# Optimization experiments

Hardware: AMD Instinct MI355X
Metric: run time of the kernel (lower is better)

The kernel has to match this reference:

```python
import jax, jax.numpy as jnp
import numpy as np

D_MODEL = 1024
NUM_HEADS = 16
D_HEAD = D_MODEL // NUM_HEADS
THETA = 10000.0
NEG_INF = -1e9


def apply_rope(x, theta=THETA):
    # x: (..., S, Dh) with interleaved pairs (2i, 2i+1)
    S, Dh = x.shape[-2], x.shape[-1]
    inv_freq = 1.0 / (theta ** (jnp.arange(0, Dh, 2, dtype=jnp.float32) / Dh))  # (Dh/2,)
    ang = jnp.arange(S, dtype=jnp.float32)[:, None] * inv_freq[None, :]          # (S, Dh/2)
    cos, sin = jnp.cos(ang), jnp.sin(ang)
    x1 = x[..., 0::2]
    x2 = x[..., 1::2]
    r1 = x1 * cos - x2 * sin
    r2 = x1 * sin + x2 * cos
    # interleave back
    return jnp.stack([r1, r2], axis=-1).reshape(x.shape)


def setup_inputs() -> dict:
    key = jax.random.key(0)
    ks = jax.random.split(key, 5)
    B, S = 2, 2048
    scale = 1.0 / np.sqrt(D_MODEL)
    return {
        "x": jax.random.normal(ks[0], (B, S, D_MODEL), dtype=jnp.float32),
        "Wq": jax.random.normal(ks[1], (D_MODEL, D_MODEL), dtype=jnp.float32) * scale,
        "Wk": jax.random.normal(ks[2], (D_MODEL, D_MODEL), dtype=jnp.float32) * scale,
        "Wv": jax.random.normal(ks[3], (D_MODEL, D_MODEL), dtype=jnp.float32) * scale,
        "Wo": jax.random.normal(ks[4], (D_MODEL, D_MODEL), dtype=jnp.float32) * scale,
    }


def reference(x, Wq, Wk, Wv, Wo):
    B, S, _ = x.shape
    def split_heads(t):
        return t.reshape(B, S, NUM_HEADS, D_HEAD).transpose(0, 2, 1, 3)  # (B,H,S,Dh)
    # nn.Linear(bias=False): y = x @ W.T
    Q = split_heads(x @ Wq.T)
    K = split_heads(x @ Wk.T)
    V = split_heads(x @ Wv.T)
    Q = apply_rope(Q)
    K = apply_rope(K)
    scale = 1.0 / jnp.sqrt(jnp.asarray(D_HEAD, dtype=x.dtype))
    scores = jnp.einsum("bhqd,bhkd->bhqk", Q, K) * scale  # (B,H,S,S)
    causal = jnp.tril(jnp.ones((S, S), dtype=bool))
    scores = jnp.where(causal, scores, NEG_INF)
    attn = jax.nn.softmax(scores, axis=-1)
    out = jnp.einsum("bhqk,bhkd->bhqd", attn, V)
    out = out.transpose(0, 2, 1, 3).reshape(B, S, D_MODEL)
    return out @ Wo.T
```

## Files before the change

### kernel.cpp

```cpp
#include <hip/hip_runtime.h>
#include <hip/hip_bf16.h>
#include <stdint.h>

typedef __attribute__((ext_vector_type(8))) short bf8;
typedef __attribute__((ext_vector_type(4))) float f4;
typedef __attribute__((ext_vector_type(16))) float f16f;
typedef __attribute__((ext_vector_type(4))) unsigned int u32x4;

#define MFMA16(a, b, c) __builtin_amdgcn_mfma_f32_16x16x32_bf16((a), (b), (c), 0, 0, 0)
#define MFMA32(a, b, c) __builtin_amdgcn_mfma_f32_32x32x16_bf16((a), (b), (c), 0, 0, 0)

static __device__ __forceinline__ short f2b(float f) {
  uint32_t x = __float_as_uint(f);
  x += 0x7fffu + ((x >> 16) & 1u);
  return (short)(x >> 16);
}

static __device__ __forceinline__ uint32_t pk2(float a, float b) {
  return ((__float_as_uint(a) + 0x8000u) >> 16) |
         ((__float_as_uint(b) + 0x8000u) & 0xffff0000u);
}

static __device__ __forceinline__ bf8 mk_bf8(uint32_t w0, uint32_t w1,
                                             uint32_t w2, uint32_t w3) {
  union { u32x4 u; bf8 b; } t;
  t.u = (u32x4){w0, w1, w2, w3};
  return t.b;
}

static __device__ __forceinline__ void gload16(const short* g, void* l) {
  __builtin_amdgcn_global_load_lds(
      (const __attribute__((address_space(1))) void*)g,
      (__attribute__((address_space(3))) void*)l, 16, 0, 0);
}

__global__ void convert_kernel(const float* __restrict__ x,
                               const float* __restrict__ wq, const float* __restrict__ wk,
                               const float* __restrict__ wv, const float* __restrict__ wo,
                               short* __restrict__ xb, short* __restrict__ Wb,
                               float2* __restrict__ tab) {
  const int bid = blockIdx.x;
  if (bid >= 4096) {
    const int t = (bid - 4096) * 256 + threadIdx.x;
    const int s = t >> 5, i = t & 31;
    const float inv = powf(10000.0f, -(float)i * (1.0f / 32.0f));
    const float ang = (float)s * inv;
    float sv, cv;
    sincosf(ang, &sv, &cv);
    tab[t] = make_float2(cv, sv);
    return;
  }
  const size_t i = ((size_t)bid * 256 + threadIdx.x) * 8;
  const float* __restrict__ src;
  short* __restrict__ dst;
  if (i < 4194304u) {
    src = x + i;
    dst = xb + i;
  } else {
    const size_t j = i - 4194304u;
    const int z = (int)(j >> 20);
    const size_t o = j & 1048575u;
    src = (z == 0 ? wq : z == 1 ? wk : z == 2 ? wv : wo) + o;
    dst = Wb + j;
  }
  const float4 a = *(const float4*)src;
  const float4 b = *(const float4*)(src + 4);
  bf8 v;
  v[0] = f2b(a.x); v[1] = f2b(a.y); v[2] = f2b(a.z); v[3] = f2b(a.w);
  v[4] = f2b(b.x); v[5] = f2b(b.y); v[6] = f2b(b.z); v[7] = f2b(b.w);
  *(bf8*)dst = v;
}

template <int MODE>
__launch_bounds__(256, 2)
__global__ void gemm_kernel(const short* __restrict__ Ab, const short* __restrict__ Wb,
                            short* __restrict__ Qo, short* __restrict__ Ko,
                            short* __restrict__ VTo, float* __restrict__ Fo,
                            const float2* __restrict__ rope) {
  constexpr int K = 1024;
  const int bm = blockIdx.x, bn = blockIdx.y;
  const int z = (MODE == 0) ? blockIdx.z : 3;
  const short* __restrict__ Bb = Wb + ((size_t)z << 20);

  __shared__ short As[128 * 64];
  __shared__ short Bs[128 * 64];

  const int tid = threadIdx.x;
  const int lane = tid & 63;
  const int wave = tid >> 6;
  const int wr = wave >> 1, wc = wave & 1;
  const int lg = lane >> 4, lr = lane & 15;

  f4 acc[4][4];
#pragma unroll
  for (int i = 0; i < 4; i++)
#pragma unroll
    for (int j = 0; j < 4; j++) {
      acc[i][j][0] = 0.f; acc[i][j][1] = 0.f;
      acc[i][j][2] = 0.f; acc[i][j][3] = 0.f;
    }

  const int kc = tid & 7;
  const int srow = tid >> 3;
  const int kcs = (kc ^ (srow & 7)) * 8;
  char* const Asw = (char*)As + wave * 1024;
  char* const Bsw = (char*)Bs + wave * 1024;

  for (int k0 = 0; k0 < K; k0 += 64) {
#pragma unroll
    for (int i = 0; i < 4; i++) {
      const int row = srow + i * 32;
      gload16(Ab + (size_t)(bm * 128 + row) * K + k0 + kcs, Asw + i * 4096);
      gload16(Bb + (size_t)(bn * 128 + row) * K + k0 + kcs, Bsw + i * 4096);
    }
    __syncthreads();
#pragma unroll
    for (int kk = 0; kk < 2; kk++) {
      bf8 af[4], bb[4];
#pragma unroll
      for (int mi = 0; mi < 4; mi++) {
        const int row = wr * 64 + mi * 16 + lr;
        const int lb = (row * 128 + kk * 64 + lg * 16) ^ ((row & 7) << 4);
        af[mi] = *(const bf8*)((const char*)As + lb);
      }
#pragma unroll
      for (int ni = 0; ni < 4; ni++) {
        const int row = wc * 64 + ni * 16 + lr;
        const int lb = (row * 128 + kk * 64 + lg * 16) ^ ((row & 7) << 4);
        bb[ni] = *(const bf8*)((const char*)Bs + lb);
      }
#pragma unroll
      for (int mi = 0; mi < 4; mi++)
#pragma unroll
        for (int ni = 0; ni < 4; ni++)
          acc[mi][ni] = MFMA16(af[mi], bb[ni], acc[mi][ni]);
    }
    __syncthreads();
  }

  if (MODE == 1) {
#pragma unroll
    for (int mi = 0; mi < 4; mi++) {
      const int m0 = bm * 128 + wr * 64 + mi * 16 + lg * 4;
#pragma unroll
      for (int ni = 0; ni < 4; ni++) {
        const int n = bn * 128 + wc * 64 + ni * 16 + lr;
#pragma unroll
        for (int r = 0; r < 4; r++)
          Fo[(size_t)(m0 + r) * 1024 + n] = acc[mi][ni][r];
      }
    }
    return;
  }

  if (z == 2) {
#pragma unroll
    for (int mi = 0; mi < 4; mi++) {
      const int m0 = bm * 128 + wr * 64 + mi * 16 + lg * 4;
      const int b = m0 >> 11, s0 = m0 & 2047;
#pragma unroll
      for (int ni = 0; ni < 4; ni++) {
        const int n = bn * 128 + wc * 64 + ni * 16 + lr;
        ushort4 pk;
        pk.x = (unsigned short)f2b(acc[mi][ni][0]);
        pk.y = (unsigned short)f2b(acc[mi][ni][1]);
        pk.z = (unsigned short)f2b(acc[mi][ni][2]);
        pk.w = (unsigned short)f2b(acc[mi][ni][3]);
        *(ushort4*)(VTo + ((size_t)((b * 16 + (n >> 6)) * 64 + (n & 63))) * 2048 + s0) = pk;
      }
    }
  } else {
    short* __restrict__ Out = (z == 0) ? Qo : Ko;
    const float qscale = (z == 0) ? 0.18033688011112042f : 1.0f;
#pragma unroll
    for (int mi = 0; mi < 4; mi++) {
      const int m0 = bm * 128 + wr * 64 + mi * 16 + lg * 4;
      const int b = m0 >> 11, s0 = m0 & 2047;
#pragma unroll
      for (int ni = 0; ni < 4; ni++) {
        const int n = bn * 128 + wc * 64 + ni * 16 + lr;
        const int h = n >> 6, d = n & 63;
        const float sgn = (d & 1) ? 1.0f : -1.0f;
#pragma unroll
        for (int r = 0; r < 4; r++) {
          const float v = acc[mi][ni][r];
          const float p = __shfl_xor(v, 1);
          const float2 cs = rope[((s0 + r) << 5) + (d >> 1)];
          const float res = (v * cs.x + sgn * p * cs.y) * qscale;
          Out[((size_t)(b * 16 + h) * 2048 + (s0 + r)) * 64 + d] = f2b(res);
        }
      }
    }
  }
}

__launch_bounds__(128, 2)
__global__ void attn_kernel(const short* __restrict__ Qg, const short* __restrict__ Kg,
                            const short* __restrict__ Vg, short* __restrict__ AO) {
  const int S = 2048;
  const int id = blockIdx.x;
  const int xcd = id & 7;
  const int rest = id >> 3;
  const int bh = xcd * 4 + (rest & 3);
  const int qt = 31 - (rest >> 2);
  const int tid = threadIdx.x;
  const int lane = tid & 63, wave = tid >> 6;
  const int l31 = lane & 31, hi = lane >> 5;
  const short* __restrict__ Qp = Qg + (size_t)bh * S * 64;
  const short* __restrict__ Kp = Kg + (size_t)bh * S * 64;
  const short* __restrict__ Vp = Vg + (size_t)bh * 64 * S;

  __shared__ short KB[2][64 * 64];
  __shared__ short VB[2][64 * 64];

  const int qbase = qt * 64 + wave * 32;
  const int nkv = qt + 1;

  const int srow = lane >> 3;
  const int chsw = ((lane & 7) ^ srow) * 8;

#define STAGE(buf, kvb_)                                                          \
  do {                                                                            \
    _Pragma("unroll") for (int c = 0; c < 4; c++) {                               \
      const int rr = wave * 32 + c * 8 + srow;                                    \
      gload16(Kp + (size_t)((kvb_) + rr) * 64 + chsw,                             \
              (char*)KB[buf] + (wave * 32 + c * 8) * 128);                        \
      gload16(Vp + (size_t)rr * 2048 + (kvb_) + chsw,                             \
              (char*)VB[buf] + (wave * 32 + c * 8) * 128);                        \
    }                                                                             \
  } while (0)

  bf8 qf[4];
#pragma unroll
  for (int ks = 0; ks < 4; ks++)
    qf[ks] = *(const bf8*)(Qp + (size_t)(qbase + l31) * 64 + ks * 16 + hi * 8);

  f16f o0, o1;
#pragma unroll
  for (int i = 0; i < 16; i++) { o0[i] = 0.f; o1[i] = 0.f; }
  float mrun = -1e30f, lsum = 0.f;

  const int rsw = (l31 & 7) << 4;

  STAGE(0, 0);
  __syncthreads();

  for (int kb = 0; kb < nkv; kb++) {
    const int kvb = kb * 64;
    const int cur = kb & 1;

    if (kb + 1 < nkv) STAGE(cur ^ 1, kvb + 64);

    const char* Kc = (const char*)KB[cur];
    const char* Vc = (const char*)VB[cur];

    f16f st0, st1;
#pragma unroll
    for (int i = 0; i < 16; i++) { st0[i] = 0.f; st1[i] = 0.f; }
    __builtin_amdgcn_s_setprio(1);
#pragma unroll
    for (int ks = 0; ks < 4; ks++) {
      const int off = ks * 32 + hi * 16;
      const bf8 k0 = *(const bf8*)(Kc + l31 * 128 + (off ^ rsw));
      const bf8 k1 = *(const bf8*)(Kc + (32 + l31) * 128 + (off ^ rsw));
      st0 = MFMA32(k0, qf[ks], st0);
      st1 = MFMA32(k1, qf[ks], st1);
    }
    __builtin_amdgcn_s_setprio(0);

    if (kvb + 63 > qbase) {
      const int q = qbase + l31;
#pragma unroll
      for (int reg = 0; reg < 16; reg++) {
        const int kv = kvb + (reg & 3) + 8 * (reg >> 2) + 4 * hi;
        if (kv > q) st0[reg] = -1e9f;
        if (kv + 32 > q) st1[reg] = -1e9f;
      }
    }

    float m0 = fmaxf(st0[0], st1[0]);
#pragma unroll
    for (int reg = 1; reg < 16; reg++) m0 = fmaxf(m0, fmaxf(st0[reg], st1[reg]));
    m0 = fmaxf(m0, __shfl_xor(m0, 32));

    if (__any(m0 - mrun > 8.0f)) {
      const float mn = fmaxf(mrun, m0);
      const float corr = __builtin_amdgcn_exp2f(mrun - mn);
      mrun = mn;
      lsum *= corr;
#pragma unroll
      for (int reg = 0; reg < 16; reg++) {
        const int qo = (reg & 3) + 8 * (reg >> 2) + 4 * hi;
        const float co = __shfl(corr, qo);
        o0[reg] *= co;
        o1[reg] *= co;
      }
    }

#pragma unroll
    for (int reg = 0; reg < 16; reg++) {
      st0[reg] = __builtin_amdgcn_exp2f(st0[reg] - mrun);
      st1[reg] = __builtin_amdgcn_exp2f(st1[reg] - mrun);
      lsum += st0[reg] + st1[reg];
    }

    bf8 pa[4];
#pragma unroll
    for (int k2 = 0; k2 < 4; k2++) {
      const f16f& pn = (k2 < 2) ? st0 : st1;
      const int bs = (k2 & 1) * 8;
      uint32_t x0 = pk2(pn[bs + 0], pn[bs + 1]);
      uint32_t y0 = pk2(pn[bs + 4], pn[bs + 5]);
      uint32_t x1 = pk2(pn[bs + 2], pn[bs + 3]);
      uint32_t y1 = pk2(pn[bs + 6], pn[bs + 7]);
      asm volatile("v_permlane32_swap_b32 %0, %1" : "+v"(x0), "+v"(y0));
      asm volatile("v_permlane32_swap_b32 %0, %1" : "+v"(x1), "+v"(y1));
      pa[k2] = mk_bf8(x0, x1, y0, y1);
    }

    __builtin_amdgcn_s_setprio(1);
#pragma unroll
    for (int k2 = 0; k2 < 4; k2++) {
      const int off = k2 * 32 + hi * 16;
      const bf8 v0 = *(const bf8*)(Vc + l31 * 128 + (off ^ rsw));
      const bf8 v1 = *(const bf8*)(Vc + (32 + l31) * 128 + (off ^ rsw));
      o0 = MFMA32(pa[k2], v0, o0);
      o1 = MFMA32(pa[k2], v1, o1);
    }
    __builtin_amdgcn_s_setprio(0);

    __syncthreads();
  }

  const float s = lsum + __shfl_xor(lsum, 32);
  const float inv = 1.0f / s;
  const int b = bh >> 4, h = bh & 15;
#pragma unroll
  for (int reg = 0; reg < 16; reg++) {
    const int qo = (reg & 3) + 8 * (reg >> 2) + 4 * hi;
    const float io = __shfl(inv, qo);
    const int q = qbase + qo;
    const size_t base = ((size_t)b * 2048 + q) * 1024 + h * 64 + l31;
    AO[base] = f2b(o0[reg] * io);
    AO[base + 32] = f2b(o1[reg] * io);
  }
#undef STAGE
}

extern "C" void kernel_launch(void* const* d_in, const int* in_sizes, int n_in,
                              void* d_out, int out_size, void* d_ws, size_t ws_size,
                              hipStream_t stream) {
  const float* x  = (const float*)d_in[0];
  const float* wq = (const float*)d_in[1];
  const float* wk = (const float*)d_in[2];
  const float* wv = (const float*)d_in[3];
  const float* wo = (const float*)d_in[4];
  float* out = (float*)d_out;

  char* ws = (char*)d_ws;
  short*  Qb  = (short*)(ws);
  short*  Kb  = (short*)(ws + (8ull  << 20));
  short*  VTb = (short*)(ws + (16ull << 20));
  short*  AOb = (short*)(ws + (24ull << 20));
  short*  xb  = AOb;
  short*  Wb  = (short*)(ws + (32ull << 20));
  float2* tab = (float2*)(ws + (40ull << 20));

  convert_kernel<<<4352, 256, 0, stream>>>(x, wq, wk, wv, wo, xb, Wb, tab);
  gemm_kernel<0><<<dim3(32, 8, 3), 256, 0, stream>>>(
      xb, Wb, Qb, Kb, VTb, nullptr, tab);
  attn_kernel<<<1024, 128, 0, stream>>>(Qb, Kb, VTb, AOb);
  gemm_kernel<1><<<dim3(32, 8, 1), 256, 0, stream>>>(
      AOb, Wb, nullptr, nullptr, nullptr, out, nullptr);
}
```

Before: 118.6 us.

## Pre-tile K and V in MFMA-ready layout and widen attention blocks to four waves

The QKV GEMM epilogue now writes K and V^T into a per-64-row tiled layout, so each attention KV tile is one contiguous 8KB chunk. That chunk can be copied straight into LDS with linear loads and needs no XOR swizzle. The attention kernel moves to 256-thread blocks with four waves covering 128 query rows, halving the block count and sharing each staged K/V tile across more waves. Waves whose causal range ends early skip compute but still join the barriers, and the unswizzled LDS reads may cause bank conflicts.

```diff
diff --git a/kernel.cpp b/kernel.cpp
--- a/kernel.cpp
+++ b/kernel.cpp
@@ -161,16 +161,17 @@
 #pragma unroll
       for (int ni = 0; ni < 4; ni++) {
         const int n = bn * 128 + wc * 64 + ni * 16 + lr;
+        const int h = n >> 6, d = n & 63;
         ushort4 pk;
         pk.x = (unsigned short)f2b(acc[mi][ni][0]);
         pk.y = (unsigned short)f2b(acc[mi][ni][1]);
         pk.z = (unsigned short)f2b(acc[mi][ni][2]);
         pk.w = (unsigned short)f2b(acc[mi][ni][3]);
-        *(ushort4*)(VTo + ((size_t)((b * 16 + (n >> 6)) * 64 + (n & 63))) * 2048 + s0) = pk;
+        ((ushort4*)VTo)[((size_t)(b * 16 + h) * 32 + (s0 >> 6)) * 1024 +
+                        (((s0 & 63) >> 2) << 6) + d] = pk;
       }
     }
   } else {
-    short* __restrict__ Out = (z == 0) ? Qo : Ko;
     const float qscale = (z == 0) ? 0.18033688011112042f : 1.0f;
 #pragma unroll
     for (int mi = 0; mi < 4; mi++) {
@@ -185,50 +186,54 @@
         for (int r = 0; r < 4; r++) {
           const float v = acc[mi][ni][r];
           const float p = __shfl_xor(v, 1);
-          const float2 cs = rope[((s0 + r) << 5) + (d >> 1)];
-          const float res = (v * cs.x + sgn * p * cs.y) * qscale;
-          Out[((size_t)(b * 16 + h) * 2048 + (s0 + r)) * 64 + d] = f2b(res);
+          const int s = s0 + r;
+          const float2 cs = rope[(s << 5) + (d >> 1)];
+          const short res = f2b((v * cs.x + sgn * p * cs.y) * qscale);
+          if (z == 0) {
+            Qo[((size_t)(b * 16 + h) * 2048 + s) * 64 + d] = res;
+          } else {
+            Ko[(((size_t)(b * 16 + h) * 32 + (s >> 6)) << 12) +
+               ((((d >> 3) << 6) + (s & 63)) << 3) + (d & 7)] = res;
+          }
         }
       }
     }
   }
 }
 
-__launch_bounds__(128, 2)
-__global__ void attn_kernel(const short* __restrict__ Qg, const short* __restrict__ Kg,
-                            const short* __restrict__ Vg, short* __restrict__ AO) {
-  const int S = 2048;
+__launch_bounds__(256, 2)
+__global__ void attn_kernel(const short* __restrict__ Qg, const short* __restrict__ K2,
+                            const short* __restrict__ V2, short* __restrict__ AO) {
   const int id = blockIdx.x;
   const int xcd = id & 7;
   const int rest = id >> 3;
   const int bh = xcd * 4 + (rest & 3);
-  const int qt = 31 - (rest >> 2);
+  const int j = 15 - (rest >> 2);
   const int tid = threadIdx.x;
   const int lane = tid & 63, wave = tid >> 6;
   const int l31 = lane & 31, hi = lane >> 5;
-  const short* __restrict__ Qp = Qg + (size_t)bh * S * 64;
-  const short* __restrict__ Kp = Kg + (size_t)bh * S * 64;
-  const short* __restrict__ Vp = Vg + (size_t)bh * 64 * S;
-
-  __shared__ short KB[2][64 * 64];
-  __shared__ short VB[2][64 * 64];
-
-  const int qbase = qt * 64 + wave * 32;
-  const int nkv = qt + 1;
-
-  const int srow = lane >> 3;
-  const int chsw = ((lane & 7) ^ srow) * 8;
-
-#define STAGE(buf, kvb_)                                                          \
-  do {                                                                            \
-    _Pragma("unroll") for (int c = 0; c < 4; c++) {                               \
-      const int rr = wave * 32 + c * 8 + srow;                                    \
-      gload16(Kp + (size_t)((kvb_) + rr) * 64 + chsw,                             \
-              (char*)KB[buf] + (wave * 32 + c * 8) * 128);                        \
-      gload16(Vp + (size_t)rr * 2048 + (kvb_) + chsw,                             \
-              (char*)VB[buf] + (wave * 32 + c * 8) * 128);                        \
-    }                                                                             \
+  const short* __restrict__ Qp = Qg + ((size_t)bh << 17);
+  const short* __restrict__ KR = K2 + ((size_t)bh << 17);
+  const short* __restrict__ VR = V2 + ((size_t)bh << 17);
+
+  __shared__ short KB[2][4096];
+  __shared__ short VB[2][4096];
+
+  const int t = 4 * j + wave;
+  const int qbase = t << 5;
+  const int my_nkv = (t >> 1) + 1;
+  const int blk_nkv = 2 * j + 2;
+
+#define STAGE(buf, kvb_)                                                       \
+  do {                                                                         \
+    const short* kr = KR + ((size_t)(kvb_) << 12);                             \
+    const short* vr = VR + ((size_t)(kvb_) << 12);                             \
+    gload16(kr + ((wave * 64) << 3), (char*)KB[buf] + wave * 1024);            \
+    gload16(kr + ((256 + wave * 64) << 3), (char*)KB[buf] + 4096 + wave * 1024); \
+    gload16(vr + ((wave * 64) << 3), (char*)VB[buf] + wave * 1024);            \
+    gload16(vr + ((256 + wave * 64) << 3), (char*)VB[buf] + 4096 + wave * 1024); \
   } while (0)
+
 
   bf8 qf[4];
 #pragma unroll
@@ -240,94 +245,111 @@
   for (int i = 0; i < 16; i++) { o0[i] = 0.f; o1[i] = 0.f; }
   float mrun = -1e30f, lsum = 0.f;
 
-  const int rsw = (l31 & 7) << 4;
-
-  STAGE(0, 0);
+  {
+    const short* kr = KR;
+    const short* vr = VR;
+    gload16(kr + (size_t)(wave * 64 + lane) * 8, (char*)KB[0] + wave * 1024);
+    gload16(kr + (size_t)(256 + wave * 64 + lane) * 8, (char*)KB[0] + 4096 + wave * 1024);
+    gload16(vr + (size_t)(wave * 64 + lane) * 8, (char*)VB[0] + wave * 1024);
+    gload16(vr + (size_t)(256 + wave * 64 + lane) * 8, (char*)VB[0] + 4096 + wave * 1024);
+  }
   __syncthreads();
 
-  for (int kb = 0; kb < nkv; kb++) {
+  for (int kb = 0; kb < blk_nkv; kb++) {
     const int kvb = kb * 64;
     const int cur = kb & 1;
 
-    if (kb + 1 < nkv) STAGE(cur ^ 1, kvb + 64);
-
-    const char* Kc = (const char*)KB[cur];
-    const char* Vc = (const char*)VB[cur];
-
-    f16f st0, st1;
-#pragma unroll
-    for (int i = 0; i < 16; i++) { st0[i] = 0.f; st1[i] = 0.f; }
-    __builtin_amdgcn_s_setprio(1);
-#pragma unroll
-    for (int ks = 0; ks < 4; ks++) {
-      const int off = ks * 32 + hi * 16;
-      const bf8 k0 = *(const bf8*)(Kc + l31 * 128 + (off ^ rsw));
-      const bf8 k1 = *(const bf8*)(Kc + (32 + l31) * 128 + (off ^ rsw));
-      st0 = MFMA32(k0, qf[ks], st0);
-      st1 = MFMA32(k1, qf[ks], st1);
-    }
-    __builtin_amdgcn_s_setprio(0);
-
-    if (kvb + 63 > qbase) {
-      const int q = qbase + l31;
+    if (kb + 1 < blk_nkv) {
+      const short* kr = KR + ((size_t)(kb + 1) << 12);
+      const short* vr = VR + ((size_t)(kb + 1) << 12);
+      gload16(kr + (size_t)(wave * 64 + lane) * 8, (char*)KB[cur ^ 1] + wave * 1024);
+      gload16(kr + (size_t)(256 + wave * 64 + lane) * 8, (char*)KB[cur ^ 1] + 4096 + wave * 1024);
+      gload16(vr + (size_t)(wave * 64 + lane) * 8, (char*)VB[cur ^ 1] + wave * 1024);
+      gload16(vr + (size_t)(256 + wave * 64 + lane) * 8, (char*)VB[cur ^ 1] + 4096 + wave * 1024);
+    }
+
+    if (kb < my_nkv) {
+      const char* Kc = (const char*)KB[cur];
+      const char* Vc = (const char*)VB[cur];
+
+      f16f st0, st1;
+#pragma unroll
+      for (int i = 0; i < 16; i++) { st0[i] = 0.f; st1[i] = 0.f; }
+      __builtin_amdgcn_s_setprio(1);
+#pragma unroll
+      for (int ks = 0; ks < 4; ks++) {
+        const bf8 k0 = *(const bf8*)(Kc + (2 * ks + hi) * 1024 + l31 * 16);
+        const bf8 k1 = *(const bf8*)(Kc + (2 * ks + hi) * 1024 + (32 + l31) * 16);
+        st0 = MFMA32(k0, qf[ks], st0);
+        st1 = MFMA32(k1, qf[ks], st1);
+      }
+      __builtin_amdgcn_s_setprio(0);
+
+      if (kvb + 63 > qbase) {
+        const int q = qbase + l31;
+#pragma unroll
+        for (int reg = 0; reg < 16; reg++) {
+          const int kv = kvb + (reg & 3) + 8 * (reg >> 2) + 4 * hi;
+          if (kv > q) st0[reg] = -1e9f;
+          if (kv + 32 > q) st1[reg] = -1e9f;
+        }
+      }
+
+      float m0 = fmaxf(st0[0], st1[0]);
+#pragma unroll
+      for (int reg = 1; reg < 16; reg++) m0 = fmaxf(m0, fmaxf(st0[reg], st1[reg]));
+      m0 = fmaxf(m0, __shfl_xor(m0, 32));
+
+      if (__any(m0 - mrun > 8.0f)) {
+        const float mn = fmaxf(mrun, m0);
+        const float corr = __builtin_amdgcn_exp2f(mrun - mn);
+        mrun = mn;
+        lsum *= corr;
+#pragma unroll
+        for (int reg = 0; reg < 16; reg++) {
+          const int qo = (reg & 3) + 8 * (reg >> 2) + 4 * hi;
+          const float co = __shfl(corr, qo);
+          o0[reg] *= co;
+          o1[reg] *= co;
+        }
+      }
+
 #pragma unroll
       for (int reg = 0; reg < 16; reg++) {
-        const int kv = kvb + (reg & 3) + 8 * (reg >> 2) + 4 * hi;
-        if (kv > q) st0[reg] = -1e9f;
-        if (kv + 32 > q) st1[reg] = -1e9f;
-      }
-    }
-
-    float m0 = fmaxf(st0[0], st1[0]);
-#pragma unroll
-    for (int reg = 1; reg < 16; reg++) m0 = fmaxf(m0, fmaxf(st0[reg], st1[reg]));
-    m0 = fmaxf(m0, __shfl_xor(m0, 32));
-
-    if (__any(m0 - mrun > 8.0f)) {
-      const float mn = fmaxf(mrun, m0);
-      const float corr = __builtin_amdgcn_exp2f(mrun - mn);
-      mrun = mn;
-      lsum *= corr;
-#pragma unroll
-      for (int reg = 0; reg < 16; reg++) {
-        const int qo = (reg & 3) + 8 * (reg >> 2) + 4 * hi;
-        const float co = __shfl(corr, qo);
-        o0[reg] *= co;
-        o1[reg] *= co;
-      }
-    }
-
-#pragma unroll
-    for (int reg = 0; reg < 16; reg++) {
-      st0[reg] = __builtin_amdgcn_exp2f(st0[reg] - mrun);
-      st1[reg] = __builtin_amdgcn_exp2f(st1[reg] - mrun);
-      lsum += st0[reg] + st1[reg];
-    }
-
-    bf8 pa[4];
-#pragma unroll
-    for (int k2 = 0; k2 < 4; k2++) {
-      const f16f& pn = (k2 < 2) ? st0 : st1;
-      const int bs = (k2 & 1) * 8;
-      uint32_t x0 = pk2(pn[bs + 0], pn[bs + 1]);
-      uint32_t y0 = pk2(pn[bs + 4], pn[bs + 5]);
-      uint32_t x1 = pk2(pn[bs + 2], pn[bs + 3]);
-      uint32_t y1 = pk2(pn[bs + 6], pn[bs + 7]);
-      asm volatile("v_permlane32_swap_b32 %0, %1" : "+v"(x0), "+v"(y0));
-      asm volatile("v_permlane32_swap_b32 %0, %1" : "+v"(x1), "+v"(y1));
-      pa[k2] = mk_bf8(x0, x1, y0, y1);
-    }
-
-    __builtin_amdgcn_s_setprio(1);
-#pragma unroll
-    for (int k2 = 0; k2 < 4; k2++) {
-      const int off = k2 * 32 + hi * 16;
-      const bf8 v0 = *(const bf8*)(Vc + l31 * 128 + (off ^ rsw));
-      const bf8 v1 = *(const bf8*)(Vc + (32 + l31) * 128 + (off ^ rsw));
-      o0 = MFMA32(pa[k2], v0, o0);
-      o1 = MFMA32(pa[k2], v1, o1);
-    }
-    __builtin_amdgcn_s_setprio(0);
+        st0[reg] = __builtin_amdgcn_exp2f(st0[reg] - mrun);
+        st1[reg] = __builtin_amdgcn_exp2f(st1[reg] - mrun);
+        lsum += st0[reg] + st1[reg];
+      }
+
+      bf8 pa[4];
+#pragma unroll
+      for (int k2 = 0; k2 < 4; k2++) {
+        const f16f& pn = (k2 < 2) ? st0 : st1;
+        const int bs = (k2 & 1) * 8;
+        uint32_t x0 = pk2(pn[bs + 0], pn[bs + 1]);
+        uint32_t y0 = pk2(pn[bs + 4], pn[bs + 5]);
+        uint32_t x1 = pk2(pn[bs + 2], pn[bs + 3]);
+        uint32_t y1 = pk2(pn[bs + 6], pn[bs + 7]);
+        asm volatile("v_permlane32_swap_b32 %0, %1" : "+v"(x0), "+v"(y0));
+        asm volatile("v_permlane32_swap_b32 %0, %1" : "+v"(x1), "+v"(y1));
+        pa[k2] = mk_bf8(x0, x1, y0, y1);
+      }
+
+      __builtin_amdgcn_s_setprio(1);
+#pragma unroll
+      for (int k2 = 0; k2 < 4; k2++) {
+        const int Jb = ((4 * k2 + 2 * hi) * 64 + l31) * 8;
+        const uint2 a0 = *(const uint2*)(Vc + Jb);
+        const uint2 a1 = *(const uint2*)(Vc + Jb + 512);
+        const uint2 b0 = *(const uint2*)(Vc + Jb + 256);
+        const uint2 b1 = *(const uint2*)(Vc + Jb + 768);
+        const bf8 v0 = mk_bf8(a0.x, a0.y, a1.x, a1.y);
+        const bf8 v1 = mk_bf8(b0.x, b0.y, b1.x, b1.y);
+        o0 = MFMA32(pa[k2], v0, o0);
+        o1 = MFMA32(pa[k2], v1, o1);
+      }
+      __builtin_amdgcn_s_setprio(0);
+    }
 
     __syncthreads();
   }
@@ -369,7 +391,7 @@
   convert_kernel<<<4352, 256, 0, stream>>>(x, wq, wk, wv, wo, xb, Wb, tab);
   gemm_kernel<0><<<dim3(32, 8, 3), 256, 0, stream>>>(
       xb, Wb, Qb, Kb, VTb, nullptr, tab);
-  attn_kernel<<<1024, 128, 0, stream>>>(Qb, Kb, VTb, AOb);
+  attn_kernel<<<512, 256, 0, stream>>>(Qb, Kb, VTb, AOb);
   gemm_kernel<1><<<dim3(32, 8, 1), 256, 0, stream>>>(
       AOb, Wb, nullptr, nullptr, nullptr, out, nullptr);
 }
```

Measured after the change: 121.6 us. 2.6% more time.
